# Performance work log

Measured on AMD Instinct MI355X. Metric: run time of the kernel, lower is better.

The kernel has to match this reference:

```python
import jax, jax.numpy as jnp
import numpy as np


def setup_inputs() -> dict:
    key = jax.random.key(0)
    ks = jax.random.split(key, 8)
    T, S, W, O = 50000, 168, 336, 48
    N = T - W - O + 1
    x = jax.random.uniform(ks[0], (T,), minval=0.5, maxval=1.5, dtype=jnp.float32)
    noise = jax.random.normal(ks[1], (N, W), dtype=jnp.float32) * 0.001  # Normal(0, std=0.001)
    level_sc = jax.random.uniform(ks[2], (), minval=-1.0, maxval=1.0, dtype=jnp.float32)
    seas_sc = jax.random.uniform(ks[3], (), minval=-1.0, maxval=1.0, dtype=jnp.float32)
    init_seas = jax.random.uniform(ks[4], (S,), minval=0.65, maxval=1.35, dtype=jnp.float32)
    W1 = jax.random.normal(ks[5], (W, W), dtype=jnp.float32) / np.float32(np.sqrt(W))
    b1 = jnp.zeros((W,), jnp.float32)
    W2 = jax.random.normal(ks[6], (W, O), dtype=jnp.float32) / np.float32(np.sqrt(W))
    b2 = jnp.zeros((O,), jnp.float32)
    return {"x": x, "noise": noise, "level_sc": level_sc, "seas_sc": seas_sc,
            "init_seas": init_seas, "W1": W1, "b1": b1, "W2": W2, "b2": b2,
            "window_size": W, "out_size": O, "lvp": 1}


def reference(x, noise, level_sc, seas_sc, init_seas, W1, b1, W2, b2,
              window_size, out_size, lvp):
    T = x.shape[0]
    a = jax.nn.sigmoid(level_sc)      # level smoothing coeff
    g = jax.nn.sigmoid(seas_sc)       # seasonal smoothing coeff
    s0 = jnp.exp(init_seas)           # [S] initial multiplicative seasonals
    # seasonals list in torch: seas[0..S-1]=s0, seas[S]=s0[0], seas[S+i]=w_i.
    # Ring buffer holds seas[i..i+S-1] at step i (starting i=1): [s0[1:], s0[0]].
    buf0 = jnp.concatenate([s0[1:], s0[:1]])
    level0 = x[0] / s0[0]

    def step(carry, xi):
        level, buf = carry
        seas_i = buf[0]
        new_level = a * xi / seas_i + (1.0 - a) * level
        new_w = g * xi / new_level + (1.0 - g) * seas_i
        new_buf = jnp.concatenate([buf[1:], new_w[None]])
        return (new_level, new_buf), (new_level, new_w, jnp.log(new_level / level))

    _, (lvls, ws, logdiffs) = jax.lax.scan(step, (level0, buf0), x[1:])
    levels = jnp.concatenate([level0[None], lvls])        # [T]
    seas_full = jnp.concatenate([s0, s0[:1], ws])         # [S+T]

    d = logdiffs[1:] - logdiffs[:-1]
    level_var_loss = jnp.mean(d * d) * lvp

    N = T - window_size - out_size + 1
    idx_in = jnp.arange(N)[:, None] + jnp.arange(window_size)[None, :]   # [N,W]
    idx_lab = jnp.arange(N)[:, None] + window_size + jnp.arange(out_size)[None, :]  # [N,O]
    lev = levels[jnp.arange(N) + window_size][:, None]    # [N,1]
    inp = jnp.log(x[idx_in] / (lev * seas_full[idx_in])) + noise   # noisy squashed inputs
    labels = jnp.log(x[idx_lab] / (lev * seas_full[idx_lab]))

    h = jnp.tanh(inp @ W1 + b1)        # tanh_no_lstm: Linear(336,336)+tanh
    out = h @ W2 + b2                  # linear_no_lstm: Linear(336,48)
    return out, labels, level_var_loss
```

## Files before the change

kernel.cpp:

```cpp
#include <hip/hip_runtime.h>

typedef __attribute__((ext_vector_type(8))) short  s16x8;
typedef __attribute__((ext_vector_type(4))) short  s16x4;
typedef __attribute__((ext_vector_type(4))) float  f32x4;

#define T_LEN 50000
#define S_LEN 168
#define W_IN  336
#define O_OUT 48
#define N_ROWS (T_LEN - W_IN - O_OUT + 1)
#define N_PAD  49664
#define NBLK   (N_PAD / 64)

__device__ inline short f2bf(float f) {
    union { float f; unsigned u; } v; v.f = f;
    unsigned u = v.u;
    unsigned r = u + 0x7fffu + ((u >> 16) & 1u);
    return (short)(r >> 16);
}

__device__ inline float readlane_f(float v, int l) {
    return __int_as_float(__builtin_amdgcn_readlane(__float_as_int(v), l));
}

__device__ inline float fast_tanh(float v) {
    float e = __expf(2.f * v);
    return 1.f - 2.f * __builtin_amdgcn_rcpf(e + 1.f);
}

__global__ void k_preconvert(const float* __restrict__ W1, const float* __restrict__ W2,
                             short* __restrict__ W1T, short* __restrict__ W2T) {
    int idx = blockIdx.x * 256 + threadIdx.x;
    const int n1 = 352 * 352;
    const int tot = n1 + 48 * 360;
    if (idx >= tot) return;
    if (idx < n1) {
        int j = idx / 352, k = idx % 352;
        W1T[idx] = (j < 336 && k < 336) ? f2bf(W1[k * 336 + j]) : (short)0;
    } else {
        int i2 = idx - n1;
        int o = i2 / 360, k = i2 % 360;
        W2T[i2] = (k < 336) ? f2bf(W2[k * 48 + o]) : (short)0;
    }
}

#define DPP_STEP(q_, CTRL, OMW) { \
    int t_ = __builtin_amdgcn_update_dpp(0, __float_as_int(q_), (CTRL), 0xf, 0xf, true); \
    q_ = fmaf((OMW), __int_as_float(t_), q_); }

__global__ void k_scan(const float* __restrict__ x, const float* __restrict__ level_sc,
                       const float* __restrict__ seas_sc, const float* __restrict__ init_seas,
                       float* __restrict__ levels, float* __restrict__ seas_full) {
    __shared__ float ring[256];
    int lane = threadIdx.x;
    float a = 1.f / (1.f + expf(-level_sc[0]));
    float g = 1.f / (1.f + expf(-seas_sc[0]));
    float om = 1.f - a, omg = 1.f - g;

    for (int t = lane; t < 256; t += 64) {
        float s = 1.f;
        if (t <= S_LEN) { s = expf(init_seas[t < S_LEN ? t : 0]); seas_full[t] = s; }
        ring[t] = s;
    }
    float lpv = x[0] / expf(init_seas[0]);
    if (lane == 0) levels[0] = lpv;
    __syncthreads();

    float om1 = om, om2v = om1 * om1, om4 = om2v * om2v, om8 = om4 * om4, om16 = om8 * om8;
    float pl   = powf(om, (float)(lane + 1));
    float fpre = powf(om, (float)((lane & 15) + 1));
    bool isr1 = (lane >> 4) == 1, isr2 = (lane >> 4) == 2, isr3 = (lane >> 4) == 3;

#define SCAN(QOUT, XV, RSV) { \
    float q_ = a * (XV) * (RSV); \
    DPP_STEP(q_, 0x111, om1); \
    DPP_STEP(q_, 0x112, om2v); \
    DPP_STEP(q_, 0x114, om4); \
    DPP_STEP(q_, 0x118, om8); \
    float e0_ = readlane_f(q_, 15); \
    float e1_ = readlane_f(q_, 31); \
    float e2_ = readlane_f(q_, 47); \
    float t2_ = fmaf(om16, e0_, e1_); \
    float t3_ = fmaf(om16, t2_, e2_); \
    float pre_ = isr1 ? e0_ : (isr2 ? t2_ : (isr3 ? t3_ : 0.f)); \
    QOUT = fmaf(fpre, pre_, q_); }

#define XLOAD(I) float xr##I = x[1 + 64 * I + lane];
    XLOAD(0) XLOAD(1) XLOAD(2) XLOAD(3) XLOAD(4) XLOAD(5) XLOAD(6) XLOAD(7)
    XLOAD(8) XLOAD(9) XLOAD(10) XLOAD(11) XLOAD(12) XLOAD(13) XLOAD(14) XLOAD(15)
#undef XLOAD

    float sA0 = ring[1 + lane];
    float Qcur; SCAN(Qcur, xr0, __builtin_amdgcn_rcpf(sA0));
    float sW = sA0;
    float ldsA = ring[65 + lane];
    float ldsB;
    int ib = 1;

#define BODY(R, RN, LIN, LOUT) { \
    float lvl = fmaf(pl, lpv, Qcur); \
    lpv = readlane_f(lvl, 63); \
    levels[ib + lane] = lvl; \
    float w_ = fmaf(omg, sW, (g * xr##R) * __builtin_amdgcn_rcpf(lvl)); \
    seas_full[S_LEN + ib + lane] = w_; \
    ring[(ib + S_LEN + lane) & 255] = w_; \
    LOUT = ring[(ib + 128 + lane) & 255]; \
    float rsn_ = __builtin_amdgcn_rcpf(LIN); \
    float Qn_; SCAN(Qn_, xr##RN, rsn_); \
    int pidx = ib + 1024 + lane; pidx = pidx > (T_LEN - 1) ? (T_LEN - 1) : pidx; \
    xr##R = x[pidx]; \
    Qcur = Qn_; sW = LIN; \
    ib += 64; }

    for (int kb = 0; kb < 48; ++kb) {
        BODY(0,1,  ldsA, ldsB) BODY(1,2,  ldsB, ldsA) BODY(2,3,  ldsA, ldsB) BODY(3,4,  ldsB, ldsA)
        BODY(4,5,  ldsA, ldsB) BODY(5,6,  ldsB, ldsA) BODY(6,7,  ldsA, ldsB) BODY(7,8,  ldsB, ldsA)
        BODY(8,9,  ldsA, ldsB) BODY(9,10, ldsB, ldsA) BODY(10,11,ldsA, ldsB) BODY(11,12,ldsB, ldsA)
        BODY(12,13,ldsA, ldsB) BODY(13,14,ldsB, ldsA) BODY(14,15,ldsA, ldsB) BODY(15,0, ldsB, ldsA)
    }
    BODY(0,1,  ldsA, ldsB) BODY(1,2,  ldsB, ldsA) BODY(2,3,  ldsA, ldsB) BODY(3,4,  ldsB, ldsA)
    BODY(4,5,  ldsA, ldsB) BODY(5,6,  ldsB, ldsA) BODY(6,7,  ldsA, ldsB) BODY(7,8,  ldsB, ldsA)
    BODY(8,9,  ldsA, ldsB) BODY(9,10, ldsB, ldsA) BODY(10,11,ldsA, ldsB) BODY(11,12,ldsB, ldsA)
#undef BODY

    {
        float lvl = fmaf(pl, lpv, Qcur);
        lpv = readlane_f(lvl, 63);
        levels[49921 + lane] = lvl;
        float w_ = fmaf(omg, sW, (g * xr12) * __builtin_amdgcn_rcpf(lvl));
        seas_full[S_LEN + 49921 + lane] = w_;
    }
    {
        float rsn_ = __builtin_amdgcn_rcpf(ldsA);
        float Qn_; SCAN(Qn_, xr13, rsn_);
        float lvl = fmaf(pl, lpv, Qn_);
        if (lane < 15) {
            levels[49985 + lane] = lvl;
            float w_ = fmaf(omg, ldsA, (g * xr13) * __builtin_amdgcn_rcpf(lvl));
            seas_full[S_LEN + 49985 + lane] = w_;
        }
    }
#undef SCAN
}

__global__ void k_logs(const float* __restrict__ x, const float* __restrict__ levels,
                       const float* __restrict__ seas_full,
                       float* __restrict__ F, float* __restrict__ llev,
                       float* __restrict__ partials) {
    __shared__ float sm[258];
    __shared__ float red[256];
    int tid = threadIdx.x;
    int t = blockIdx.x * 256 + tid;
    float ll = 0.f;
    if (t < T_LEN) {
        F[t]  = __logf(x[t]) - __logf(seas_full[t]);
        ll    = __logf(levels[t]);
        llev[t] = ll;
    }
    sm[tid] = ll;
    if (tid < 2) {
        int te = blockIdx.x * 256 + 256 + tid;
        sm[256 + tid] = (te < T_LEN) ? __logf(levels[te]) : 0.f;
    }
    __syncthreads();
    float s = 0.f;
    if (t < T_LEN - 2) {
        float d = sm[tid + 2] - 2.f * sm[tid + 1] + sm[tid];
        s = d * d;
    }
    red[tid] = s; __syncthreads();
    for (int off = 128; off > 0; off >>= 1) {
        if (tid < off) red[tid] += red[tid + off];
        __syncthreads();
    }
    if (tid == 0) partials[blockIdx.x] = red[0];
}

__global__ __launch_bounds__(256, 3) void k_gemm(
        const float* __restrict__ noise, const float* __restrict__ F,
        const float* __restrict__ llev, const short* __restrict__ W1T,
        const float* __restrict__ b1, const short* __restrict__ W2T,
        const float* __restrict__ b2, const float* __restrict__ partials,
        const int* __restrict__ lvp, float* __restrict__ out,
        float* __restrict__ labels, float* __restrict__ loss) {
    __shared__ __align__(16) short hlds[64][360];
    __shared__ __align__(16) float Flds[448];
    __shared__ __align__(16) float Llds[64];
    __shared__ __align__(16) float b1lds[352];

    int t = threadIdx.x, w = t >> 6, l = t & 63;
    int lm = l & 15, lq = l >> 4;
    long n0 = (long)blockIdx.x * 64;

    if (blockIdx.x == 0 && w == 3) {
        float s = partials[l] + partials[l + 64] + partials[l + 128];
        if (l < 4) s += partials[l + 192];
#pragma unroll
        for (int off = 32; off > 0; off >>= 1) s += __shfl_down(s, off, 64);
        if (l == 0) loss[0] = s / (float)(T_LEN - 2) * (float)lvp[0];
    }

    if (t < 112)      *(f32x4*)&Flds[t * 4] = *(const f32x4*)&F[n0 + t * 4];
    else if (t < 128) *(f32x4*)&Llds[(t - 112) * 4] = *(const f32x4*)&llev[n0 + W_IN + (t - 112) * 4];
    else if (t < 216) {
        int i4 = (t - 128) * 4;
        f32x4 v = (f32x4){0.f, 0.f, 0.f, 0.f};
        if (i4 < W_IN) v = *(const f32x4*)&b1[i4];
        *(f32x4*)&b1lds[i4] = v;
    }

    int rbase = (w >> 1) * 32;
    int jbase = (w & 1) * 176;
    long an0 = n0 + rbase + lm, an1 = an0 + 16;
    const long amax = (long)N_ROWS * W_IN - 8;
    long a00 = an0 * W_IN, a10 = an1 * W_IN;

    long p0 = a00 + lq * 8; if (p0 > amax) p0 = amax;
    long p1 = a10 + lq * 8; if (p1 > amax) p1 = amax;
    f32x4 nc00 = *(const f32x4*)&noise[p0], nc01 = *(const f32x4*)&noise[p0 + 4];
    f32x4 nc10 = *(const f32x4*)&noise[p1], nc11 = *(const f32x4*)&noise[p1 + 4];

    f32x4 acc0[11], acc1[11];
#pragma unroll
    for (int c = 0; c < 11; ++c) { acc0[c] = (f32x4){0,0,0,0}; acc1[c] = (f32x4){0,0,0,0}; }

    __syncthreads();
    float lv0 = Llds[rbase + lm], lv1 = Llds[rbase + 16 + lm];

    const short* w1row = &W1T[(jbase + lm) * 352 + lq * 8];
#define LDW(CT) (*(const s16x8*)&w1row[(CT) * 16 * 352 + ks * 32])
#pragma unroll 1
    for (int ks = 0; ks < 11; ++ks) {
        int fb = rbase + lm + ks * 32 + lq * 8;
        s16x8 bf0, bf1;
#pragma unroll
        for (int j = 0; j < 8; ++j) {
            float nv0 = (j < 4) ? nc00[j] : nc01[j - 4];
            float nv1 = (j < 4) ? nc10[j] : nc11[j - 4];
            bf0[j] = f2bf(Flds[fb + j]      - lv0 + nv0);
            bf1[j] = f2bf(Flds[fb + 16 + j] - lv1 + nv1);
        }
        if (ks < 10) {
            int kb = (ks + 1) * 32 + lq * 8;
            long q0 = a00 + kb; if (q0 > amax) q0 = amax;
            long q1 = a10 + kb; if (q1 > amax) q1 = amax;
            nc00 = *(const f32x4*)&noise[q0]; nc01 = *(const f32x4*)&noise[q0 + 4];
            nc10 = *(const f32x4*)&noise[q1]; nc11 = *(const f32x4*)&noise[q1 + 4];
        }
        s16x8 af0 = LDW(0), af1 = LDW(1), af2 = LDW(2);
#define MM2(CT, AF) \
        acc0[CT] = __builtin_amdgcn_mfma_f32_16x16x32_bf16(AF, bf0, acc0[CT], 0, 0, 0); \
        acc1[CT] = __builtin_amdgcn_mfma_f32_16x16x32_bf16(AF, bf1, acc1[CT], 0, 0, 0);
        MM2(0, af0)  af0 = LDW(3);
        MM2(1, af1)  af1 = LDW(4);
        MM2(2, af2)  af2 = LDW(5);
        MM2(3, af0)  af0 = LDW(6);
        MM2(4, af1)  af1 = LDW(7);
        MM2(5, af2)  af2 = LDW(8);
        MM2(6, af0)  af0 = LDW(9);
        MM2(7, af1)  af1 = LDW(10);
        MM2(8, af2)
        MM2(9, af0)
        MM2(10, af1)
#undef MM2
    }
#undef LDW

#pragma unroll
    for (int ct = 0; ct < 11; ++ct) {
        f32x4 b1q = *(f32x4*)&b1lds[jbase + ct * 16 + lq * 4];
        s16x4 h0, h1;
#pragma unroll
        for (int r = 0; r < 4; ++r) {
            h0[r] = f2bf(fast_tanh(acc0[ct][r] + b1q[r]));
            h1[r] = f2bf(fast_tanh(acc1[ct][r] + b1q[r]));
        }
        *(s16x4*)&hlds[rbase + lm][jbase + ct * 16 + lq * 4]      = h0;
        *(s16x4*)&hlds[rbase + 16 + lm][jbase + ct * 16 + lq * 4] = h1;
    }
    __syncthreads();

    f32x4 a2[3];
    a2[0] = (f32x4){0,0,0,0}; a2[1] = (f32x4){0,0,0,0}; a2[2] = (f32x4){0,0,0,0};
#pragma unroll
    for (int ks = 0; ks < 11; ++ks) {
        s16x8 af2 = *(s16x8*)&hlds[w * 16 + lm][ks * 32 + lq * 8];
#pragma unroll
        for (int ct = 0; ct < 3; ++ct) {
            s16x8 bf2 = *(const s16x8*)&W2T[(ct * 16 + lm) * 360 + ks * 32 + lq * 8];
            a2[ct] = __builtin_amdgcn_mfma_f32_16x16x32_bf16(af2, bf2, a2[ct], 0, 0, 0);
        }
    }

    int rloc = w * 16 + lq * 4;
#pragma unroll
    for (int ct = 0; ct < 3; ++ct) {
        float b2v = b2[ct * 16 + lm];
#pragma unroll
        for (int r = 0; r < 4; ++r) {
            long row = n0 + rloc + r;
            if (row < N_ROWS) {
                int col = ct * 16 + lm;
                out[row * O_OUT + col]    = a2[ct][r] + b2v;
                labels[row * O_OUT + col] = Flds[rloc + r + W_IN + col] - Llds[rloc + r];
            }
        }
    }
}

extern "C" void kernel_launch(void* const* d_in, const int* in_sizes, int n_in,
                              void* d_out, int out_size, void* d_ws, size_t ws_size,
                              hipStream_t stream) {
    const float* x         = (const float*)d_in[0];
    const float* noise     = (const float*)d_in[1];
    const float* level_sc  = (const float*)d_in[2];
    const float* seas_sc   = (const float*)d_in[3];
    const float* init_seas = (const float*)d_in[4];
    const float* W1        = (const float*)d_in[5];
    const float* b1        = (const float*)d_in[6];
    const float* W2        = (const float*)d_in[7];
    const float* b2        = (const float*)d_in[8];
    const int*   lvp       = (const int*)d_in[11];

    float* out    = (float*)d_out;
    float* labels = out + (long)N_ROWS * O_OUT;
    float* loss   = labels + (long)N_ROWS * O_OUT;

    float* wsf       = (float*)d_ws;
    float* levels    = wsf;
    float* seas_full = wsf + 50048;
    float* F         = wsf + 100224;
    float* llev      = wsf + 150400;
    float* partials  = wsf + 200448;
    short* W1T       = (short*)(wsf + 200704);
    short* W2T       = W1T + 352 * 352;

    k_preconvert<<<552, 256, 0, stream>>>(W1, W2, W1T, W2T);
    k_scan<<<1, 64, 0, stream>>>(x, level_sc, seas_sc, init_seas, levels, seas_full);
    k_logs<<<196, 256, 0, stream>>>(x, levels, seas_full, F, llev, partials);
    k_gemm<<<NBLK, 256, 0, stream>>>(noise, F, llev, W1T, b1, W2T, b2,
                                     partials, lvp, out, labels, loss);
}
```

Measured before the change: 156.0 us.

## Shorten scan critical path, pack scan stores, fully unroll GEMM with prefetch

The serial scan now merges its cross-row prefix with two more row-broadcast DPP FMA steps instead of readlanes and a select chain. It writes level and seasonal as one interleaved float2 store and applies the index clamp only in the last iterations. The first GEMM loop is fully unrolled: all 11 W1 fragments stay in registers and are prefetched one k-step ahead, and noise is double-buffered two steps ahead. BF16 conversion uses packed float2-to-bf16 intrinsics. These changes target the latency of the single-wave scan and the memory stalls in the GEMM, at the cost of higher register pressure in k_gemm.

```diff
diff --git a/kernel.cpp b/kernel.cpp
--- a/kernel.cpp
+++ b/kernel.cpp
@@ -1,4 +1,5 @@
 #include <hip/hip_runtime.h>
+#include <hip/hip_bf16.h>
 
 typedef __attribute__((ext_vector_type(8))) short  s16x8;
 typedef __attribute__((ext_vector_type(4))) short  s16x4;
@@ -17,6 +18,13 @@
     unsigned u = v.u;
     unsigned r = u + 0x7fffu + ((u >> 16) & 1u);
     return (short)(r >> 16);
+}
+
+__device__ inline int bfpk(float lo, float hi) {
+    float2 f2; f2.x = lo; f2.y = hi;
+    __hip_bfloat162 h = __float22bfloat162_rn(f2);
+    int r; __builtin_memcpy(&r, &h, 4);
+    return r;
 }
 
 __device__ inline float readlane_f(float v, int l) {
@@ -44,13 +52,13 @@
     }
 }
 
-#define DPP_STEP(q_, CTRL, OMW) { \
-    int t_ = __builtin_amdgcn_update_dpp(0, __float_as_int(q_), (CTRL), 0xf, 0xf, true); \
-    q_ = fmaf((OMW), __int_as_float(t_), q_); }
+#define DPP_FMA(q_, CTRL, W, RM) { \
+    int t_ = __builtin_amdgcn_update_dpp(0, __float_as_int(q_), (CTRL), (RM), 0xf, true); \
+    q_ = fmaf((W), __int_as_float(t_), q_); }
 
 __global__ void k_scan(const float* __restrict__ x, const float* __restrict__ level_sc,
                        const float* __restrict__ seas_sc, const float* __restrict__ init_seas,
-                       float* __restrict__ levels, float* __restrict__ seas_full) {
+                       float* __restrict__ lw, float* __restrict__ seasinit) {
     __shared__ float ring[256];
     int lane = threadIdx.x;
     float a = 1.f / (1.f + expf(-level_sc[0]));
@@ -59,31 +67,27 @@
 
     for (int t = lane; t < 256; t += 64) {
         float s = 1.f;
-        if (t <= S_LEN) { s = expf(init_seas[t < S_LEN ? t : 0]); seas_full[t] = s; }
+        if (t <= S_LEN) { s = expf(init_seas[t < S_LEN ? t : 0]); seasinit[t] = s; }
         ring[t] = s;
     }
     float lpv = x[0] / expf(init_seas[0]);
-    if (lane == 0) levels[0] = lpv;
+    if (lane == 0) { lw[0] = lpv; lw[1] = 1.f; }
     __syncthreads();
 
-    float om1 = om, om2v = om1 * om1, om4 = om2v * om2v, om8 = om4 * om4, om16 = om8 * om8;
-    float pl   = powf(om, (float)(lane + 1));
-    float fpre = powf(om, (float)((lane & 15) + 1));
-    bool isr1 = (lane >> 4) == 1, isr2 = (lane >> 4) == 2, isr3 = (lane >> 4) == 3;
+    float om1 = om, om2v = om1 * om1, om4 = om2v * om2v, om8 = om4 * om4;
+    float pl    = powf(om, (float)(lane + 1));
+    float fpre  = powf(om, (float)((lane & 15) + 1));
+    float fpre2 = powf(om, (float)((lane & 31) + 1));
 
 #define SCAN(QOUT, XV, RSV) { \
     float q_ = a * (XV) * (RSV); \
-    DPP_STEP(q_, 0x111, om1); \
-    DPP_STEP(q_, 0x112, om2v); \
-    DPP_STEP(q_, 0x114, om4); \
-    DPP_STEP(q_, 0x118, om8); \
-    float e0_ = readlane_f(q_, 15); \
-    float e1_ = readlane_f(q_, 31); \
-    float e2_ = readlane_f(q_, 47); \
-    float t2_ = fmaf(om16, e0_, e1_); \
-    float t3_ = fmaf(om16, t2_, e2_); \
-    float pre_ = isr1 ? e0_ : (isr2 ? t2_ : (isr3 ? t3_ : 0.f)); \
-    QOUT = fmaf(fpre, pre_, q_); }
+    DPP_FMA(q_, 0x111, om1,  0xf); \
+    DPP_FMA(q_, 0x112, om2v, 0xf); \
+    DPP_FMA(q_, 0x114, om4,  0xf); \
+    DPP_FMA(q_, 0x118, om8,  0xf); \
+    DPP_FMA(q_, 0x142, fpre,  0xa); \
+    DPP_FMA(q_, 0x143, fpre2, 0xc); \
+    QOUT = q_; }
 
 #define XLOAD(I) float xr##I = x[1 + 64 * I + lane];
     XLOAD(0) XLOAD(1) XLOAD(2) XLOAD(3) XLOAD(4) XLOAD(5) XLOAD(6) XLOAD(7)
@@ -97,54 +101,58 @@
     float ldsB;
     int ib = 1;
 
-#define BODY(R, RN, LIN, LOUT) { \
+#define BODY(R, RN, LIN, LOUT, CLAMP) { \
     float lvl = fmaf(pl, lpv, Qcur); \
     lpv = readlane_f(lvl, 63); \
-    levels[ib + lane] = lvl; \
     float w_ = fmaf(omg, sW, (g * xr##R) * __builtin_amdgcn_rcpf(lvl)); \
-    seas_full[S_LEN + ib + lane] = w_; \
+    float2 pk_; pk_.x = lvl; pk_.y = w_; \
+    *(float2*)&lw[2 * (ib + lane)] = pk_; \
     ring[(ib + S_LEN + lane) & 255] = w_; \
     LOUT = ring[(ib + 128 + lane) & 255]; \
-    float rsn_ = __builtin_amdgcn_rcpf(LIN); \
-    float Qn_; SCAN(Qn_, xr##RN, rsn_); \
-    int pidx = ib + 1024 + lane; pidx = pidx > (T_LEN - 1) ? (T_LEN - 1) : pidx; \
+    float Qn_; SCAN(Qn_, xr##RN, __builtin_amdgcn_rcpf(LIN)); \
+    int pidx = ib + 1024 + lane; \
+    if (CLAMP) pidx = pidx > (T_LEN - 1) ? (T_LEN - 1) : pidx; \
     xr##R = x[pidx]; \
     Qcur = Qn_; sW = LIN; \
     ib += 64; }
 
-    for (int kb = 0; kb < 48; ++kb) {
-        BODY(0,1,  ldsA, ldsB) BODY(1,2,  ldsB, ldsA) BODY(2,3,  ldsA, ldsB) BODY(3,4,  ldsB, ldsA)
-        BODY(4,5,  ldsA, ldsB) BODY(5,6,  ldsB, ldsA) BODY(6,7,  ldsA, ldsB) BODY(7,8,  ldsB, ldsA)
-        BODY(8,9,  ldsA, ldsB) BODY(9,10, ldsB, ldsA) BODY(10,11,ldsA, ldsB) BODY(11,12,ldsB, ldsA)
-        BODY(12,13,ldsA, ldsB) BODY(13,14,ldsB, ldsA) BODY(14,15,ldsA, ldsB) BODY(15,0, ldsB, ldsA)
-    }
-    BODY(0,1,  ldsA, ldsB) BODY(1,2,  ldsB, ldsA) BODY(2,3,  ldsA, ldsB) BODY(3,4,  ldsB, ldsA)
-    BODY(4,5,  ldsA, ldsB) BODY(5,6,  ldsB, ldsA) BODY(6,7,  ldsA, ldsB) BODY(7,8,  ldsB, ldsA)
-    BODY(8,9,  ldsA, ldsB) BODY(9,10, ldsB, ldsA) BODY(10,11,ldsA, ldsB) BODY(11,12,ldsB, ldsA)
+    for (int kb = 0; kb < 47; ++kb) {
+        BODY(0,1,  ldsA, ldsB, 0) BODY(1,2,  ldsB, ldsA, 0) BODY(2,3,  ldsA, ldsB, 0) BODY(3,4,  ldsB, ldsA, 0)
+        BODY(4,5,  ldsA, ldsB, 0) BODY(5,6,  ldsB, ldsA, 0) BODY(6,7,  ldsA, ldsB, 0) BODY(7,8,  ldsB, ldsA, 0)
+        BODY(8,9,  ldsA, ldsB, 0) BODY(9,10, ldsB, ldsA, 0) BODY(10,11,ldsA, ldsB, 0) BODY(11,12,ldsB, ldsA, 0)
+        BODY(12,13,ldsA, ldsB, 0) BODY(13,14,ldsB, ldsA, 0) BODY(14,15,ldsA, ldsB, 0) BODY(15,0, ldsB, ldsA, 0)
+    }
+    BODY(0,1,  ldsA, ldsB, 0) BODY(1,2,  ldsB, ldsA, 0) BODY(2,3,  ldsA, ldsB, 0) BODY(3,4,  ldsB, ldsA, 0)
+    BODY(4,5,  ldsA, ldsB, 0) BODY(5,6,  ldsB, ldsA, 0) BODY(6,7,  ldsA, ldsB, 0) BODY(7,8,  ldsB, ldsA, 0)
+    BODY(8,9,  ldsA, ldsB, 0) BODY(9,10, ldsB, ldsA, 0) BODY(10,11,ldsA, ldsB, 0) BODY(11,12,ldsB, ldsA, 0)
+    BODY(12,13,ldsA, ldsB, 0)
+    BODY(13,14,ldsB, ldsA, 1) BODY(14,15,ldsA, ldsB, 1) BODY(15,0, ldsB, ldsA, 1)
+    BODY(0,1,  ldsA, ldsB, 1) BODY(1,2,  ldsB, ldsA, 1) BODY(2,3,  ldsA, ldsB, 1) BODY(3,4,  ldsB, ldsA, 1)
+    BODY(4,5,  ldsA, ldsB, 1) BODY(5,6,  ldsB, ldsA, 1) BODY(6,7,  ldsA, ldsB, 1) BODY(7,8,  ldsB, ldsA, 1)
+    BODY(8,9,  ldsA, ldsB, 1) BODY(9,10, ldsB, ldsA, 1) BODY(10,11,ldsA, ldsB, 1) BODY(11,12,ldsB, ldsA, 1)
 #undef BODY
 
     {
         float lvl = fmaf(pl, lpv, Qcur);
         lpv = readlane_f(lvl, 63);
-        levels[49921 + lane] = lvl;
         float w_ = fmaf(omg, sW, (g * xr12) * __builtin_amdgcn_rcpf(lvl));
-        seas_full[S_LEN + 49921 + lane] = w_;
+        float2 pk_; pk_.x = lvl; pk_.y = w_;
+        *(float2*)&lw[2 * (49921 + lane)] = pk_;
     }
     {
-        float rsn_ = __builtin_amdgcn_rcpf(ldsA);
-        float Qn_; SCAN(Qn_, xr13, rsn_);
+        float Qn_; SCAN(Qn_, xr13, __builtin_amdgcn_rcpf(ldsA));
         float lvl = fmaf(pl, lpv, Qn_);
         if (lane < 15) {
-            levels[49985 + lane] = lvl;
             float w_ = fmaf(omg, ldsA, (g * xr13) * __builtin_amdgcn_rcpf(lvl));
-            seas_full[S_LEN + 49985 + lane] = w_;
+            float2 pk_; pk_.x = lvl; pk_.y = w_;
+            *(float2*)&lw[2 * (49985 + lane)] = pk_;
         }
     }
 #undef SCAN
 }
 
-__global__ void k_logs(const float* __restrict__ x, const float* __restrict__ levels,
-                       const float* __restrict__ seas_full,
+__global__ void k_logs(const float* __restrict__ x, const float* __restrict__ lw,
+                       const float* __restrict__ seasinit,
                        float* __restrict__ F, float* __restrict__ llev,
                        float* __restrict__ partials) {
     __shared__ float sm[258];
@@ -153,14 +161,17 @@
     int t = blockIdx.x * 256 + tid;
     float ll = 0.f;
     if (t < T_LEN) {
-        F[t]  = __logf(x[t]) - __logf(seas_full[t]);
-        ll    = __logf(levels[t]);
+        float2 cur = *(const float2*)&lw[2 * t];
+        int ps = t - S_LEN; if (ps < 0) ps = 0;
+        float sv = (t <= S_LEN) ? seasinit[t] : lw[2 * ps + 1];
+        F[t]  = __logf(x[t]) - __logf(sv);
+        ll    = __logf(cur.x);
         llev[t] = ll;
     }
     sm[tid] = ll;
     if (tid < 2) {
         int te = blockIdx.x * 256 + 256 + tid;
-        sm[256 + tid] = (te < T_LEN) ? __logf(levels[te]) : 0.f;
+        sm[256 + tid] = (te < T_LEN) ? __logf(lw[2 * te]) : 0.f;
     }
     __syncthreads();
     float s = 0.f;
@@ -215,68 +226,84 @@
     const long amax = (long)N_ROWS * W_IN - 8;
     long a00 = an0 * W_IN, a10 = an1 * W_IN;
 
-    long p0 = a00 + lq * 8; if (p0 > amax) p0 = amax;
-    long p1 = a10 + lq * 8; if (p1 > amax) p1 = amax;
-    f32x4 nc00 = *(const f32x4*)&noise[p0], nc01 = *(const f32x4*)&noise[p0 + 4];
-    f32x4 nc10 = *(const f32x4*)&noise[p1], nc11 = *(const f32x4*)&noise[p1 + 4];
+    f32x4 ncE00, ncE01, ncE10, ncE11, ncO00, ncO01, ncO10, ncO11;
+    {
+        long p0 = a00 + lq * 8; if (p0 > amax) p0 = amax;
+        long p1 = a10 + lq * 8; if (p1 > amax) p1 = amax;
+        ncE00 = *(const f32x4*)&noise[p0]; ncE01 = *(const f32x4*)&noise[p0 + 4];
+        ncE10 = *(const f32x4*)&noise[p1]; ncE11 = *(const f32x4*)&noise[p1 + 4];
+        long q0 = a00 + 32 + lq * 8; if (q0 > amax) q0 = amax;
+        long q1 = a10 + 32 + lq * 8; if (q1 > amax) q1 = amax;
+        ncO00 = *(const f32x4*)&noise[q0]; ncO01 = *(const f32x4*)&noise[q0 + 4];
+        ncO10 = *(const f32x4*)&noise[q1]; ncO11 = *(const f32x4*)&noise[q1 + 4];
+    }
 
     f32x4 acc0[11], acc1[11];
 #pragma unroll
     for (int c = 0; c < 11; ++c) { acc0[c] = (f32x4){0,0,0,0}; acc1[c] = (f32x4){0,0,0,0}; }
+
+    const short* w1row = &W1T[(jbase + lm) * 352 + lq * 8];
+#define LDW(CT, KS) (*(const s16x8*)&w1row[(CT) * 5632 + (KS) * 32])
+    s16x8 af0 = LDW(0,0), af1 = LDW(1,0), af2 = LDW(2,0), af3 = LDW(3,0), af4 = LDW(4,0),
+          af5 = LDW(5,0), af6 = LDW(6,0), af7 = LDW(7,0), af8 = LDW(8,0), af9 = LDW(9,0),
+          af10 = LDW(10,0);
 
     __syncthreads();
     float lv0 = Llds[rbase + lm], lv1 = Llds[rbase + 16 + lm];
 
-    const short* w1row = &W1T[(jbase + lm) * 352 + lq * 8];
-#define LDW(CT) (*(const s16x8*)&w1row[(CT) * 16 * 352 + ks * 32])
-#pragma unroll 1
-    for (int ks = 0; ks < 11; ++ks) {
-        int fb = rbase + lm + ks * 32 + lq * 8;
-        s16x8 bf0, bf1;
-#pragma unroll
-        for (int j = 0; j < 8; ++j) {
-            float nv0 = (j < 4) ? nc00[j] : nc01[j - 4];
-            float nv1 = (j < 4) ? nc10[j] : nc11[j - 4];
-            bf0[j] = f2bf(Flds[fb + j]      - lv0 + nv0);
-            bf1[j] = f2bf(Flds[fb + 16 + j] - lv1 + nv1);
-        }
-        if (ks < 10) {
-            int kb = (ks + 1) * 32 + lq * 8;
-            long q0 = a00 + kb; if (q0 > amax) q0 = amax;
-            long q1 = a10 + kb; if (q1 > amax) q1 = amax;
-            nc00 = *(const f32x4*)&noise[q0]; nc01 = *(const f32x4*)&noise[q0 + 4];
-            nc10 = *(const f32x4*)&noise[q1]; nc11 = *(const f32x4*)&noise[q1 + 4];
-        }
-        s16x8 af0 = LDW(0), af1 = LDW(1), af2 = LDW(2);
 #define MM2(CT, AF) \
-        acc0[CT] = __builtin_amdgcn_mfma_f32_16x16x32_bf16(AF, bf0, acc0[CT], 0, 0, 0); \
-        acc1[CT] = __builtin_amdgcn_mfma_f32_16x16x32_bf16(AF, bf1, acc1[CT], 0, 0, 0);
-        MM2(0, af0)  af0 = LDW(3);
-        MM2(1, af1)  af1 = LDW(4);
-        MM2(2, af2)  af2 = LDW(5);
-        MM2(3, af0)  af0 = LDW(6);
-        MM2(4, af1)  af1 = LDW(7);
-        MM2(5, af2)  af2 = LDW(8);
-        MM2(6, af0)  af0 = LDW(9);
-        MM2(7, af1)  af1 = LDW(10);
-        MM2(8, af2)
-        MM2(9, af0)
-        MM2(10, af1)
+    acc0[CT] = __builtin_amdgcn_mfma_f32_16x16x32_bf16(AF, bf0, acc0[CT], 0, 0, 0); \
+    acc1[CT] = __builtin_amdgcn_mfma_f32_16x16x32_bf16(AF, bf1, acc1[CT], 0, 0, 0);
+
+#define KSTEP(KS, NCX) { \
+    s16x8 bf0, bf1; \
+    { int fb = rbase + lm + (KS) * 32 + lq * 8; \
+      int* b0i = (int*)&bf0; int* b1i = (int*)&bf1; \
+      b0i[0] = bfpk(Flds[fb+0]  - lv0 + NCX##00[0], Flds[fb+1]  - lv0 + NCX##00[1]); \
+      b0i[1] = bfpk(Flds[fb+2]  - lv0 + NCX##00[2], Flds[fb+3]  - lv0 + NCX##00[3]); \
+      b0i[2] = bfpk(Flds[fb+4]  - lv0 + NCX##01[0], Flds[fb+5]  - lv0 + NCX##01[1]); \
+      b0i[3] = bfpk(Flds[fb+6]  - lv0 + NCX##01[2], Flds[fb+7]  - lv0 + NCX##01[3]); \
+      b1i[0] = bfpk(Flds[fb+16] - lv1 + NCX##10[0], Flds[fb+17] - lv1 + NCX##10[1]); \
+      b1i[1] = bfpk(Flds[fb+18] - lv1 + NCX##10[2], Flds[fb+19] - lv1 + NCX##10[3]); \
+      b1i[2] = bfpk(Flds[fb+20] - lv1 + NCX##11[0], Flds[fb+21] - lv1 + NCX##11[1]); \
+      b1i[3] = bfpk(Flds[fb+22] - lv1 + NCX##11[2], Flds[fb+23] - lv1 + NCX##11[3]); } \
+    if ((KS) + 2 <= 10) { \
+      int kb = ((KS) + 2) * 32 + lq * 8; \
+      long q0 = a00 + kb; if (q0 > amax) q0 = amax; \
+      long q1 = a10 + kb; if (q1 > amax) q1 = amax; \
+      NCX##00 = *(const f32x4*)&noise[q0]; NCX##01 = *(const f32x4*)&noise[q0 + 4]; \
+      NCX##10 = *(const f32x4*)&noise[q1]; NCX##11 = *(const f32x4*)&noise[q1 + 4]; \
+    } \
+    MM2(0, af0)   if ((KS) < 10) af0  = LDW(0,  (KS) + 1); \
+    MM2(1, af1)   if ((KS) < 10) af1  = LDW(1,  (KS) + 1); \
+    MM2(2, af2)   if ((KS) < 10) af2  = LDW(2,  (KS) + 1); \
+    MM2(3, af3)   if ((KS) < 10) af3  = LDW(3,  (KS) + 1); \
+    MM2(4, af4)   if ((KS) < 10) af4  = LDW(4,  (KS) + 1); \
+    MM2(5, af5)   if ((KS) < 10) af5  = LDW(5,  (KS) + 1); \
+    MM2(6, af6)   if ((KS) < 10) af6  = LDW(6,  (KS) + 1); \
+    MM2(7, af7)   if ((KS) < 10) af7  = LDW(7,  (KS) + 1); \
+    MM2(8, af8)   if ((KS) < 10) af8  = LDW(8,  (KS) + 1); \
+    MM2(9, af9)   if ((KS) < 10) af9  = LDW(9,  (KS) + 1); \
+    MM2(10, af10) if ((KS) < 10) af10 = LDW(10, (KS) + 1); \
+}
+
+    KSTEP(0, ncE) KSTEP(1, ncO) KSTEP(2, ncE) KSTEP(3, ncO) KSTEP(4, ncE)
+    KSTEP(5, ncO) KSTEP(6, ncE) KSTEP(7, ncO) KSTEP(8, ncE) KSTEP(9, ncO)
+    KSTEP(10, ncE)
+#undef KSTEP
 #undef MM2
-    }
 #undef LDW
 
 #pragma unroll
     for (int ct = 0; ct < 11; ++ct) {
         f32x4 b1q = *(f32x4*)&b1lds[jbase + ct * 16 + lq * 4];
-        s16x4 h0, h1;
-#pragma unroll
-        for (int r = 0; r < 4; ++r) {
-            h0[r] = f2bf(fast_tanh(acc0[ct][r] + b1q[r]));
-            h1[r] = f2bf(fast_tanh(acc1[ct][r] + b1q[r]));
-        }
-        *(s16x4*)&hlds[rbase + lm][jbase + ct * 16 + lq * 4]      = h0;
-        *(s16x4*)&hlds[rbase + 16 + lm][jbase + ct * 16 + lq * 4] = h1;
+        int2 p0, p1;
+        p0.x = bfpk(fast_tanh(acc0[ct][0] + b1q[0]), fast_tanh(acc0[ct][1] + b1q[1]));
+        p0.y = bfpk(fast_tanh(acc0[ct][2] + b1q[2]), fast_tanh(acc0[ct][3] + b1q[3]));
+        p1.x = bfpk(fast_tanh(acc1[ct][0] + b1q[0]), fast_tanh(acc1[ct][1] + b1q[1]));
+        p1.y = bfpk(fast_tanh(acc1[ct][2] + b1q[2]), fast_tanh(acc1[ct][3] + b1q[3]));
+        *(int2*)&hlds[rbase + lm][jbase + ct * 16 + lq * 4]      = p0;
+        *(int2*)&hlds[rbase + 16 + lm][jbase + ct * 16 + lq * 4] = p1;
     }
     __syncthreads();
 
@@ -284,11 +311,11 @@
     a2[0] = (f32x4){0,0,0,0}; a2[1] = (f32x4){0,0,0,0}; a2[2] = (f32x4){0,0,0,0};
 #pragma unroll
     for (int ks = 0; ks < 11; ++ks) {
-        s16x8 af2 = *(s16x8*)&hlds[w * 16 + lm][ks * 32 + lq * 8];
+        s16x8 hf = *(s16x8*)&hlds[w * 16 + lm][ks * 32 + lq * 8];
 #pragma unroll
         for (int ct = 0; ct < 3; ++ct) {
             s16x8 bf2 = *(const s16x8*)&W2T[(ct * 16 + lm) * 360 + ks * 32 + lq * 8];
-            a2[ct] = __builtin_amdgcn_mfma_f32_16x16x32_bf16(af2, bf2, a2[ct], 0, 0, 0);
+            a2[ct] = __builtin_amdgcn_mfma_f32_16x16x32_bf16(hf, bf2, a2[ct], 0, 0, 0);
         }
     }
 
@@ -326,18 +353,18 @@
     float* labels = out + (long)N_ROWS * O_OUT;
     float* loss   = labels + (long)N_ROWS * O_OUT;
 
-    float* wsf       = (float*)d_ws;
-    float* levels    = wsf;
-    float* seas_full = wsf + 50048;
-    float* F         = wsf + 100224;
-    float* llev      = wsf + 150400;
-    float* partials  = wsf + 200448;
-    short* W1T       = (short*)(wsf + 200704);
-    short* W2T       = W1T + 352 * 352;
+    float* wsf      = (float*)d_ws;
+    float* lw       = wsf;
+    float* seasinit = wsf + 100096;
+    float* F        = wsf + 100288;
+    float* llev     = wsf + 150464;
+    float* partials = wsf + 200512;
+    short* W1T      = (short*)(wsf + 200768);
+    short* W2T      = W1T + 352 * 352;
 
     k_preconvert<<<552, 256, 0, stream>>>(W1, W2, W1T, W2T);
-    k_scan<<<1, 64, 0, stream>>>(x, level_sc, seas_sc, init_seas, levels, seas_full);
-    k_logs<<<196, 256, 0, stream>>>(x, levels, seas_full, F, llev, partials);
+    k_scan<<<1, 64, 0, stream>>>(x, level_sc, seas_sc, init_seas, lw, seasinit);
+    k_logs<<<196, 256, 0, stream>>>(x, lw, seasinit, F, llev, partials);
     k_gemm<<<NBLK, 256, 0, stream>>>(noise, F, llev, W1T, b1, W2T, b2,
                                      partials, lvp, out, labels, loss);
 }
```

Result: slower. 165.3 us (+6.0%).
